# Performance work log

Hardware: AMD Instinct MI355X
Metric: run time of the kernel (lower is better)

The kernel has to match this reference:

```python
import jax, jax.numpy as jnp
import numpy as np

B, C, H, Wd, IN_CAPS = 128, 32, 12, 12, 8
OUT_CH, OUT_CAPS, ROUTING_ITERS = 10, 16, 3


def setup_inputs() -> dict:
    key = jax.random.key(0)
    k1, k2 = jax.random.split(key)
    x = jax.random.normal(k1, (B, C, H, Wd, IN_CAPS), dtype=jnp.float32)
    W = jax.random.normal(k2, (1, 1, C, OUT_CH, OUT_CAPS, IN_CAPS), dtype=jnp.float32)
    return {"x": x, "W": W}


def _squash(s):
    # s: [..., out_caps]
    sn = jnp.sum(s * s, axis=-1, keepdims=True)
    return sn * s / ((1.0 + sn) * jnp.sqrt(sn))


def reference(x, W):
    b = x.shape[0]
    # [B, H, W, C, in_caps]
    u = jnp.transpose(x, (0, 2, 3, 1, 4))
    Wm = W[0, 0]  # [C, out_ch, out_caps, in_caps]
    # u_hat[b,h,w,c,o,p] = sum_q Wm[c,o,p,q] * u[b,h,w,c,q]
    u_hat = jnp.einsum('copq,bhwcq->bhwcop', Wm, u)
    u_hat = u_hat.reshape(b, -1, OUT_CH, OUT_CAPS)  # [B, N, O, P]

    b_ij = jnp.zeros(u_hat.shape[:-1], dtype=u_hat.dtype)  # [B, N, O]
    v_j = None
    for i in range(ROUTING_ITERS):
        c_ij = jax.nn.softmax(b_ij, axis=-1)[..., None]  # [B, N, O, 1]
        s_j = jnp.sum(c_ij * u_hat, axis=1)              # [B, O, P]
        v_j = _squash(s_j)                               # [B, O, P]
        if i < ROUTING_ITERS - 1:
            a_j = jnp.sum(u_hat * v_j[:, None], axis=-1)  # [B, N, O]
            b_ij = b_ij + a_j
    return v_j
```

## Files before the change

kernel.cpp:

```cpp
#include <hip/hip_runtime.h>


#define BB 128
#define CC 32
#define HWN 144
#define QQ 8
#define OO 10
#define PP 16

__global__ __launch_bounds__(256, 1)
void digitcaps_routing(const float* __restrict__ x, const float* __restrict__ Wm,
                       float* __restrict__ out) {
    const int b    = blockIdx.x;
    const int tid  = threadIdx.x;
    const int c    = tid >> 3;
    const int slot = tid & 7;

    __shared__ float usum_s[CC * QQ];
    __shared__ float Wv_s[CC * OO * QQ];
    __shared__ float t_s[CC * OO * QQ];
    __shared__ float v_s[OO * PP];

    const float* xb = x + (size_t)b * (CC * HWN * QQ);
    const float* xc = xb + c * (HWN * QQ);

    float us[QQ];
#pragma unroll
    for (int q = 0; q < QQ; ++q) us[q] = 0.f;
#pragma unroll
    for (int i = 0; i < 18; ++i) {
        const int hw = slot + (i << 3);
        const float4* p4 = (const float4*)(xc + hw * QQ);
        float4 a = p4[0], d = p4[1];
        us[0] += a.x; us[1] += a.y; us[2] += a.z; us[3] += a.w;
        us[4] += d.x; us[5] += d.y; us[6] += d.z; us[7] += d.w;
    }
#pragma unroll
    for (int m = 1; m <= 4; m <<= 1) {
#pragma unroll
        for (int q = 0; q < QQ; ++q) us[q] += __shfl_xor(us[q], m);
    }
    if (slot == 0) {
#pragma unroll
        for (int q = 0; q < QQ; ++q) usum_s[c * QQ + q] = us[q];
    }
    __syncthreads();

    if (tid < OO * PP) {
        const int o = tid >> 4, p = tid & 15;
        float s = 0.f;
        for (int cc = 0; cc < CC; ++cc) {
            const float4* w4 = (const float4*)(Wm + (((cc * OO + o) * PP + p) * QQ));
            float4 w0 = w4[0], w1 = w4[1];
            const float* u0 = &usum_s[cc * QQ];
            s += w0.x * u0[0] + w0.y * u0[1] + w0.z * u0[2] + w0.w * u0[3]
               + w1.x * u0[4] + w1.y * u0[5] + w1.z * u0[6] + w1.w * u0[7];
        }
        s *= 0.1f;
        float sn = s * s;
#pragma unroll
        for (int m = 1; m <= 8; m <<= 1) sn += __shfl_xor(sn, m);
        const float fac = sqrtf(sn) / (1.f + sn);
        v_s[tid] = s * fac;
    }
    for (int k = tid; k < CC * OO * QQ; k += 256) Wv_s[k] = 0.f;
    __syncthreads();

    for (int iter = 0; iter < 2; ++iter) {
        for (int k = tid; k < CC * OO * QQ; k += 256) {
            const int cc  = k / (OO * QQ);
            const int rem = k - cc * (OO * QQ);
            const int o   = rem >> 3, q = rem & 7;
            const float* wp = Wm + ((cc * OO + o) * PP) * QQ + q;
            float acc = 0.f;
#pragma unroll
            for (int p = 0; p < PP; ++p) acc += wp[p * QQ] * v_s[o * PP + p];
            Wv_s[k] += acc;
        }
        __syncthreads();

        float wv[OO][QQ];
#pragma unroll
        for (int o = 0; o < OO; ++o)
#pragma unroll
            for (int q = 0; q < QQ; ++q) wv[o][q] = Wv_s[(c * OO + o) * QQ + q];

        float tl[OO][QQ];
#pragma unroll
        for (int o = 0; o < OO; ++o)
#pragma unroll
            for (int q = 0; q < QQ; ++q) tl[o][q] = 0.f;

        for (int i = 0; i < 18; ++i) {
            const int hw = slot + (i << 3);
            const float4* p4 = (const float4*)(xc + hw * QQ);
            float4 a = p4[0], d = p4[1];
            float u[QQ] = {a.x, a.y, a.z, a.w, d.x, d.y, d.z, d.w};
            float lg[OO];
            float mx = -1e30f;
#pragma unroll
            for (int o = 0; o < OO; ++o) {
                float t = 0.f;
#pragma unroll
                for (int q = 0; q < QQ; ++q) t += u[q] * wv[o][q];
                lg[o] = t;
                mx = fmaxf(mx, t);
            }
            float ssum = 0.f;
#pragma unroll
            for (int o = 0; o < OO; ++o) { lg[o] = __expf(lg[o] - mx); ssum += lg[o]; }
            const float inv = 1.f / ssum;
#pragma unroll
            for (int o = 0; o < OO; ++o) {
                const float cij = lg[o] * inv;
#pragma unroll
                for (int q = 0; q < QQ; ++q) tl[o][q] += cij * u[q];
            }
        }
#pragma unroll
        for (int m = 1; m <= 4; m <<= 1) {
#pragma unroll
            for (int o = 0; o < OO; ++o)
#pragma unroll
                for (int q = 0; q < QQ; ++q) tl[o][q] += __shfl_xor(tl[o][q], m);
        }
        if (slot == 0) {
#pragma unroll
            for (int o = 0; o < OO; ++o)
#pragma unroll
                for (int q = 0; q < QQ; ++q) t_s[(c * OO + o) * QQ + q] = tl[o][q];
        }
        __syncthreads();

        if (tid < OO * PP) {
            const int o = tid >> 4, p = tid & 15;
            float s = 0.f;
            for (int cc = 0; cc < CC; ++cc) {
                const float4* w4 = (const float4*)(Wm + (((cc * OO + o) * PP + p) * QQ));
                float4 w0 = w4[0], w1 = w4[1];
                const float* t0 = &t_s[(cc * OO + o) * QQ];
                s += w0.x * t0[0] + w0.y * t0[1] + w0.z * t0[2] + w0.w * t0[3]
                   + w1.x * t0[4] + w1.y * t0[5] + w1.z * t0[6] + w1.w * t0[7];
            }
            float sn = s * s;
#pragma unroll
            for (int m = 1; m <= 8; m <<= 1) sn += __shfl_xor(sn, m);
            const float fac = sqrtf(sn) / (1.f + sn);
            const float v = s * fac;
            if (iter == 1) out[(size_t)b * (OO * PP) + tid] = v;
            else           v_s[tid] = v;
        }
        __syncthreads();
    }
}

extern "C" void kernel_launch(void* const* d_in, const int* in_sizes, int n_in,
                              void* d_out, int out_size, void* d_ws, size_t ws_size,
                              hipStream_t stream) {
    const float* x  = (const float*)d_in[0];
    const float* Wm = (const float*)d_in[1];
    float* out = (float*)d_out;
    digitcaps_routing<<<BB, 256, 0, stream>>>(x, Wm, out);
}
```

Measured before the change: 103.5 us.

## Split routing into multiple kernels with spatial chunking across blocks

Replaces the single one-block-per-batch kernel with an init kernel, a heavy routing kernel gridded over batch and six spatial chunks, and a reduction kernel that sums the chunk partials and updates Wv. Partial sums and Wv now live in global device buffers. The aim is to fill the GPU with 768 blocks instead of 128. The cost is five launches and extra global-memory traffic between stages.

Result: slower. 120.0 us (+15.9%).

```diff
diff --git a/kernel.cpp b/kernel.cpp
--- a/kernel.cpp
+++ b/kernel.cpp
@@ -7,36 +7,33 @@
 #define QQ 8
 #define OO 10
 #define PP 16
-
-__global__ __launch_bounds__(256, 1)
-void digitcaps_routing(const float* __restrict__ x, const float* __restrict__ Wm,
-                       float* __restrict__ out) {
-    const int b    = blockIdx.x;
-    const int tid  = threadIdx.x;
-    const int c    = tid >> 3;
-    const int slot = tid & 7;
-
+#define NCH 6
+#define CHW 24
+
+__device__ float g_Wv[BB * CC * OO * QQ];
+__device__ float g_ps[BB * NCH * OO * PP];
+
+__global__ __launch_bounds__(512, 1)
+void k_init(const float* __restrict__ x, const float* __restrict__ Wm) {
+    const int b = blockIdx.x, tid = threadIdx.x;
+    const int c = tid >> 4, slot = tid & 15;
     __shared__ float usum_s[CC * QQ];
-    __shared__ float Wv_s[CC * OO * QQ];
-    __shared__ float t_s[CC * OO * QQ];
     __shared__ float v_s[OO * PP];
 
-    const float* xb = x + (size_t)b * (CC * HWN * QQ);
-    const float* xc = xb + c * (HWN * QQ);
-
+    const float* xc = x + ((size_t)b * CC + c) * (HWN * QQ);
     float us[QQ];
 #pragma unroll
     for (int q = 0; q < QQ; ++q) us[q] = 0.f;
 #pragma unroll
-    for (int i = 0; i < 18; ++i) {
-        const int hw = slot + (i << 3);
+    for (int i = 0; i < 9; ++i) {
+        const int hw = slot + (i << 4);
         const float4* p4 = (const float4*)(xc + hw * QQ);
         float4 a = p4[0], d = p4[1];
         us[0] += a.x; us[1] += a.y; us[2] += a.z; us[3] += a.w;
         us[4] += d.x; us[5] += d.y; us[6] += d.z; us[7] += d.w;
     }
 #pragma unroll
-    for (int m = 1; m <= 4; m <<= 1) {
+    for (int m = 1; m <= 8; m <<= 1) {
 #pragma unroll
         for (int q = 0; q < QQ; ++q) us[q] += __shfl_xor(us[q], m);
     }
@@ -63,94 +60,148 @@
         const float fac = sqrtf(sn) / (1.f + sn);
         v_s[tid] = s * fac;
     }
-    for (int k = tid; k < CC * OO * QQ; k += 256) Wv_s[k] = 0.f;
     __syncthreads();
 
-    for (int iter = 0; iter < 2; ++iter) {
-        for (int k = tid; k < CC * OO * QQ; k += 256) {
-            const int cc  = k / (OO * QQ);
-            const int rem = k - cc * (OO * QQ);
-            const int o   = rem >> 3, q = rem & 7;
-            const float* wp = Wm + ((cc * OO + o) * PP) * QQ + q;
-            float acc = 0.f;
-#pragma unroll
-            for (int p = 0; p < PP; ++p) acc += wp[p * QQ] * v_s[o * PP + p];
-            Wv_s[k] += acc;
-        }
+    if (tid < CC * OO) {
+        const int o = tid >> 5, cc = tid & 31;
+        float acc[QQ];
+#pragma unroll
+        for (int q = 0; q < QQ; ++q) acc[q] = 0.f;
+        const float* wp = Wm + ((cc * OO + o) * PP) * QQ;
+#pragma unroll
+        for (int p = 0; p < PP; ++p) {
+            const float vv = v_s[o * PP + p];
+            const float4* w4 = (const float4*)(wp + p * QQ);
+            float4 w0 = w4[0], w1 = w4[1];
+            acc[0] += vv * w0.x; acc[1] += vv * w0.y; acc[2] += vv * w0.z; acc[3] += vv * w0.w;
+            acc[4] += vv * w1.x; acc[5] += vv * w1.y; acc[6] += vv * w1.z; acc[7] += vv * w1.w;
+        }
+        float* wvp = g_Wv + (size_t)b * (CC * OO * QQ);
+#pragma unroll
+        for (int q = 0; q < QQ; ++q) wvp[(o * QQ + q) * CC + cc] = acc[q];
+    }
+}
+
+__global__ __launch_bounds__(256, 3)
+void k_heavy(const float* __restrict__ x, const float* __restrict__ Wm) {
+    const int chunk = blockIdx.x;
+    const int b     = blockIdx.y;
+    const int tid   = threadIdx.x;
+    const int c     = tid >> 3;
+    const int slot  = tid & 7;
+
+    __shared__ float t_s[CC * OO * QQ];
+
+    const float* wvb = g_Wv + (size_t)b * (CC * OO * QQ);
+    float wv[OO][QQ];
+#pragma unroll
+    for (int o = 0; o < OO; ++o)
+#pragma unroll
+        for (int q = 0; q < QQ; ++q) wv[o][q] = wvb[(o * QQ + q) * CC + c];
+
+    const float* xc = x + ((size_t)b * CC + c) * (HWN * QQ);
+    float tl[OO][QQ];
+#pragma unroll
+    for (int o = 0; o < OO; ++o)
+#pragma unroll
+        for (int q = 0; q < QQ; ++q) tl[o][q] = 0.f;
+
+#pragma unroll
+    for (int i = 0; i < 3; ++i) {
+        const int hw = chunk * CHW + slot + (i << 3);
+        const float4* p4 = (const float4*)(xc + hw * QQ);
+        float4 a = p4[0], d = p4[1];
+        float u[QQ] = {a.x, a.y, a.z, a.w, d.x, d.y, d.z, d.w};
+        float lg[OO];
+        float mx = -1e30f;
+#pragma unroll
+        for (int o = 0; o < OO; ++o) {
+            float t = 0.f;
+#pragma unroll
+            for (int q = 0; q < QQ; ++q) t += u[q] * wv[o][q];
+            lg[o] = t;
+            mx = fmaxf(mx, t);
+        }
+        float ssum = 0.f;
+#pragma unroll
+        for (int o = 0; o < OO; ++o) { lg[o] = __expf(lg[o] - mx); ssum += lg[o]; }
+        const float inv = 1.f / ssum;
+#pragma unroll
+        for (int o = 0; o < OO; ++o) {
+            const float cij = lg[o] * inv;
+#pragma unroll
+            for (int q = 0; q < QQ; ++q) tl[o][q] += cij * u[q];
+        }
+    }
+#pragma unroll
+    for (int m = 1; m <= 4; m <<= 1) {
+#pragma unroll
+        for (int o = 0; o < OO; ++o)
+#pragma unroll
+            for (int q = 0; q < QQ; ++q) tl[o][q] += __shfl_xor(tl[o][q], m);
+    }
+    if (slot == 0) {
+#pragma unroll
+        for (int o = 0; o < OO; ++o)
+#pragma unroll
+            for (int q = 0; q < QQ; ++q) t_s[c * (OO * QQ) + o * QQ + q] = tl[o][q];
+    }
+    __syncthreads();
+
+    if (tid < OO * PP) {
+        const int o = tid >> 4, p = tid & 15;
+        float s = 0.f;
+        for (int cc = 0; cc < CC; ++cc) {
+            const float4* w4 = (const float4*)(Wm + (((cc * OO + o) * PP + p) * QQ));
+            float4 w0 = w4[0], w1 = w4[1];
+            const float4* t4 = (const float4*)(t_s + cc * (OO * QQ) + o * QQ);
+            float4 t0 = t4[0], t1 = t4[1];
+            s += w0.x * t0.x + w0.y * t0.y + w0.z * t0.z + w0.w * t0.w
+               + w1.x * t1.x + w1.y * t1.y + w1.z * t1.z + w1.w * t1.w;
+        }
+        g_ps[((size_t)b * NCH + chunk) * (OO * PP) + tid] = s;
+    }
+}
+
+template <int FINAL>
+__global__ __launch_bounds__(320, 1)
+void k_red(const float* __restrict__ Wm, float* __restrict__ out) {
+    const int b = blockIdx.x, tid = threadIdx.x;
+    __shared__ float v_s[OO * PP];
+
+    if (tid < OO * PP) {
+        float s = 0.f;
+#pragma unroll
+        for (int ch = 0; ch < NCH; ++ch)
+            s += g_ps[((size_t)b * NCH + ch) * (OO * PP) + tid];
+        float sn = s * s;
+#pragma unroll
+        for (int m = 1; m <= 8; m <<= 1) sn += __shfl_xor(sn, m);
+        const float fac = sqrtf(sn) / (1.f + sn);
+        const float v = s * fac;
+        if (FINAL) out[(size_t)b * (OO * PP) + tid] = v;
+        else       v_s[tid] = v;
+    }
+    if (!FINAL) {
         __syncthreads();
-
-        float wv[OO][QQ];
-#pragma unroll
-        for (int o = 0; o < OO; ++o)
-#pragma unroll
-            for (int q = 0; q < QQ; ++q) wv[o][q] = Wv_s[(c * OO + o) * QQ + q];
-
-        float tl[OO][QQ];
-#pragma unroll
-        for (int o = 0; o < OO; ++o)
-#pragma unroll
-            for (int q = 0; q < QQ; ++q) tl[o][q] = 0.f;
-
-        for (int i = 0; i < 18; ++i) {
-            const int hw = slot + (i << 3);
-            const float4* p4 = (const float4*)(xc + hw * QQ);
-            float4 a = p4[0], d = p4[1];
-            float u[QQ] = {a.x, a.y, a.z, a.w, d.x, d.y, d.z, d.w};
-            float lg[OO];
-            float mx = -1e30f;
-#pragma unroll
-            for (int o = 0; o < OO; ++o) {
-                float t = 0.f;
-#pragma unroll
-                for (int q = 0; q < QQ; ++q) t += u[q] * wv[o][q];
-                lg[o] = t;
-                mx = fmaxf(mx, t);
+        if (tid < CC * OO) {
+            const int o = tid >> 5, cc = tid & 31;
+            float acc[QQ];
+#pragma unroll
+            for (int q = 0; q < QQ; ++q) acc[q] = 0.f;
+            const float* wp = Wm + ((cc * OO + o) * PP) * QQ;
+#pragma unroll
+            for (int p = 0; p < PP; ++p) {
+                const float vv = v_s[o * PP + p];
+                const float4* w4 = (const float4*)(wp + p * QQ);
+                float4 w0 = w4[0], w1 = w4[1];
+                acc[0] += vv * w0.x; acc[1] += vv * w0.y; acc[2] += vv * w0.z; acc[3] += vv * w0.w;
+                acc[4] += vv * w1.x; acc[5] += vv * w1.y; acc[6] += vv * w1.z; acc[7] += vv * w1.w;
             }
-            float ssum = 0.f;
-#pragma unroll
-            for (int o = 0; o < OO; ++o) { lg[o] = __expf(lg[o] - mx); ssum += lg[o]; }
-            const float inv = 1.f / ssum;
-#pragma unroll
-            for (int o = 0; o < OO; ++o) {
-                const float cij = lg[o] * inv;
-#pragma unroll
-                for (int q = 0; q < QQ; ++q) tl[o][q] += cij * u[q];
-            }
-        }
-#pragma unroll
-        for (int m = 1; m <= 4; m <<= 1) {
-#pragma unroll
-            for (int o = 0; o < OO; ++o)
-#pragma unroll
-                for (int q = 0; q < QQ; ++q) tl[o][q] += __shfl_xor(tl[o][q], m);
-        }
-        if (slot == 0) {
-#pragma unroll
-            for (int o = 0; o < OO; ++o)
-#pragma unroll
-                for (int q = 0; q < QQ; ++q) t_s[(c * OO + o) * QQ + q] = tl[o][q];
-        }
-        __syncthreads();
-
-        if (tid < OO * PP) {
-            const int o = tid >> 4, p = tid & 15;
-            float s = 0.f;
-            for (int cc = 0; cc < CC; ++cc) {
-                const float4* w4 = (const float4*)(Wm + (((cc * OO + o) * PP + p) * QQ));
-                float4 w0 = w4[0], w1 = w4[1];
-                const float* t0 = &t_s[(cc * OO + o) * QQ];
-                s += w0.x * t0[0] + w0.y * t0[1] + w0.z * t0[2] + w0.w * t0[3]
-                   + w1.x * t0[4] + w1.y * t0[5] + w1.z * t0[6] + w1.w * t0[7];
-            }
-            float sn = s * s;
-#pragma unroll
-            for (int m = 1; m <= 8; m <<= 1) sn += __shfl_xor(sn, m);
-            const float fac = sqrtf(sn) / (1.f + sn);
-            const float v = s * fac;
-            if (iter == 1) out[(size_t)b * (OO * PP) + tid] = v;
-            else           v_s[tid] = v;
-        }
-        __syncthreads();
+            float* wvp = g_Wv + (size_t)b * (CC * OO * QQ);
+#pragma unroll
+            for (int q = 0; q < QQ; ++q) wvp[(o * QQ + q) * CC + cc] += acc[q];
+        }
     }
 }
 
@@ -160,5 +211,10 @@
     const float* x  = (const float*)d_in[0];
     const float* Wm = (const float*)d_in[1];
     float* out = (float*)d_out;
-    digitcaps_routing<<<BB, 256, 0, stream>>>(x, Wm, out);
-}
+
+    k_init<<<dim3(BB), dim3(512), 0, stream>>>(x, Wm);
+    k_heavy<<<dim3(NCH, BB), dim3(256), 0, stream>>>(x, Wm);
+    k_red<0><<<dim3(BB), dim3(320), 0, stream>>>(Wm, out);
+    k_heavy<<<dim3(NCH, BB), dim3(256), 0, stream>>>(x, Wm);
+    k_red<1><<<dim3(BB), dim3(320), 0, stream>>>(Wm, out);
+}
```
